# Kernel tuning notes

Measured on AMD Instinct MI355X. Metric: run time of the kernel, lower is better.

Reference implementation:

```python
import jax, jax.numpy as jnp
import numpy as np

B, T, D_IN, H1, H2 = 32, 2048, 1024, 512, 32


def setup_inputs() -> dict:
    key = jax.random.key(0)
    ks = jax.random.split(key, 8)
    avf_out = jax.random.normal(ks[0], (B, T, D_IN), dtype=jnp.float32)
    # seq_len in [1, T] so every sample has a non-empty slice (matches torch usage)
    seq_len = jax.random.randint(ks[1], (B,), 1, T + 1, dtype=jnp.int32)
    s = 0.02
    W1 = jax.random.normal(ks[2], (D_IN, H1), dtype=jnp.float32) * s
    b1 = jnp.zeros((H1,), dtype=jnp.float32)
    W2 = jax.random.normal(ks[3], (H1, H2), dtype=jnp.float32) * s
    b2 = jnp.zeros((H2,), dtype=jnp.float32)
    W3 = jax.random.normal(ks[4], (H2, 1), dtype=jnp.float32) * s
    b3 = jnp.zeros((1,), dtype=jnp.float32)
    return {"avf_out": avf_out, "W1": W1, "b1": b1, "W2": W2, "b2": b2,
            "W3": W3, "b3": b3, "seq_len": seq_len}


def reference(avf_out, W1, b1, W2, b2, W3, b3, seq_len):
    h = jax.nn.relu(jnp.einsum('btd,dh->bth', avf_out, W1) + b1)
    h = jnp.einsum('bth,hk->btk', h, W2) + b2
    logits = jax.nn.sigmoid(jnp.einsum('btk,ko->bto', h, W3) + b3)[..., 0]  # [B, T]
    # ragged per-sample top-k (k = seq_len//16 + 1 over first seq_len entries) + mean,
    # vectorized via masked descending sort + cumsum (no per-sample loop)
    Tn = logits.shape[1]
    valid = jnp.arange(Tn)[None, :] < seq_len[:, None]            # [B, T]
    NEG = jnp.float32(-1.0)  # below sigmoid range, so padded slots never enter top-k
    masked = jnp.where(valid, logits, NEG)
    sorted_desc = -jnp.sort(-masked, axis=1)                      # [B, T] descending
    csum = jnp.cumsum(sorted_desc, axis=1)
    k = seq_len // 16 + 1                                         # k <= seq_len always
    topk_sum = jnp.take_along_axis(csum, (k - 1)[:, None].astype(jnp.int32), axis=1)[:, 0]
    return topk_sum / k.astype(logits.dtype)                      # [B]
```

## Files before the change

kernel.cpp:

```cpp
#include <hip/hip_runtime.h>

typedef __bf16 bf16;
typedef __bf16 bf16x4 __attribute__((ext_vector_type(4)));
typedef __bf16 bf16x8 __attribute__((ext_vector_type(8)));
typedef float f32x4 __attribute__((ext_vector_type(4)));

#define M_TOT 65536
#define K_TOT 1024
#define N_TOT 512
#define T_SEQ 2048
#define NB 32

__device__ __forceinline__ void async16(const void* g, void* l) {
    __builtin_amdgcn_global_load_lds(
        (const __attribute__((address_space(1))) unsigned int*)g,
        (__attribute__((address_space(3))) unsigned int*)l, 16, 0, 0);
}

__global__ __launch_bounds__(256) void transpose_w1(const float* __restrict__ W1,
                                                    bf16* __restrict__ W1T) {
    __shared__ float tile[32][33];
    const int t = threadIdx.x;
    const int k0 = blockIdx.x * 32;
    const int n0 = blockIdx.y * 32;
#pragma unroll
    for (int p = 0; p < 4; p++) {
        int kl = p * 8 + (t >> 5);
        int nl = t & 31;
        tile[kl][nl] = W1[(k0 + kl) * 512 + n0 + nl];
    }
    __syncthreads();
#pragma unroll
    for (int p = 0; p < 4; p++) {
        int nl = p * 8 + (t >> 5);
        int kl = t & 31;
        W1T[(n0 + nl) * 1024 + k0 + kl] = (bf16)tile[kl][nl];
    }
}

__global__ __launch_bounds__(512) void make_v(const float* __restrict__ W2,
                                              const float* __restrict__ b2,
                                              const float* __restrict__ W3,
                                              const float* __restrict__ b3,
                                              float* __restrict__ v) {
    const int t = threadIdx.x;
    float s = 0.f;
#pragma unroll
    for (int c = 0; c < 32; c++) s += W2[t * 32 + c] * W3[c];
    v[t] = s;
    if (t == 0) {
        float cc = b3[0];
        for (int c = 0; c < 32; c++) cc += b2[c] * W3[c];
        v[512] = cc;
    }
}

__device__ __forceinline__ int sw_idx(int row, int e) {
    return row * 64 + ((((e >> 3) ^ (row & 7))) << 3) + (e & 7);
}

__global__ __launch_bounds__(512, 1) void gemm_fused(const float* __restrict__ A,
                                                     const bf16* __restrict__ W1T,
                                                     const float* __restrict__ b1,
                                                     const float* __restrict__ v,
                                                     float* __restrict__ logits) {
    __shared__ bf16 smem[(128 + 512) * 64];
    bf16* As = smem;
    bf16* Bs = smem + 128 * 64;

    const int t = threadIdx.x;
    const int wave = t >> 6, lane = t & 63;
    const int q = lane >> 4, l15 = lane & 15;
    const int wm = wave >> 2, wn = wave & 3;
    const int m0 = blockIdx.x * 128;

    const int arow = t >> 2;
    const int ae0  = (t & 3) * 16;
    const float* agp = A + (size_t)(m0 + arow) * K_TOT + ae0;

    const int bl_row   = wave * 64 + (lane >> 3);
    const int bl_chunk = (lane & 7) ^ ((lane >> 3) & 7);
    const bf16* bgp = W1T + (size_t)bl_row * K_TOT + bl_chunk * 8;

    f32x4 acc[4][8] = {};

#pragma unroll 1
    for (int k0 = 0; k0 < K_TOT; k0 += 64) {
        float4 av[4];
#pragma unroll
        for (int p = 0; p < 4; p++) av[p] = *(const float4*)(agp + k0 + p * 4);

        __syncthreads();

#pragma unroll
        for (int j = 0; j < 8; j++)
            async16(bgp + k0 + (size_t)j * 8 * K_TOT,
                    Bs + (wave * 64 + j * 8) * 64);

        {
            bf16x8 c0, c1;
            c0[0] = (bf16)av[0].x; c0[1] = (bf16)av[0].y;
            c0[2] = (bf16)av[0].z; c0[3] = (bf16)av[0].w;
            c0[4] = (bf16)av[1].x; c0[5] = (bf16)av[1].y;
            c0[6] = (bf16)av[1].z; c0[7] = (bf16)av[1].w;
            c1[0] = (bf16)av[2].x; c1[1] = (bf16)av[2].y;
            c1[2] = (bf16)av[2].z; c1[3] = (bf16)av[2].w;
            c1[4] = (bf16)av[3].x; c1[5] = (bf16)av[3].y;
            c1[6] = (bf16)av[3].z; c1[7] = (bf16)av[3].w;
            *(bf16x8*)(&As[sw_idx(arow, ae0)])     = c0;
            *(bf16x8*)(&As[sw_idx(arow, ae0 + 8)]) = c1;
        }

        __syncthreads();

#pragma unroll
        for (int kk = 0; kk < 64; kk += 32) {
            const int e = kk + q * 8;
            bf16x8 af[4], bfr[8];
#pragma unroll
            for (int mi = 0; mi < 4; mi++) {
                int row = wm * 64 + mi * 16 + l15;
                af[mi] = *(const bf16x8*)(&As[sw_idx(row, e)]);
            }
#pragma unroll
            for (int ni = 0; ni < 8; ni++) {
                int n = wn * 128 + ni * 16 + l15;
                bfr[ni] = *(const bf16x8*)(&Bs[sw_idx(n, e)]);
            }
#pragma unroll
            for (int mi = 0; mi < 4; mi++)
#pragma unroll
                for (int ni = 0; ni < 8; ni++)
                    acc[mi][ni] = __builtin_amdgcn_mfma_f32_16x16x32_bf16(
                        af[mi], bfr[ni], acc[mi][ni], 0, 0, 0);
        }
    }

    float bb[8], vv[8];
#pragma unroll
    for (int ni = 0; ni < 8; ni++) {
        int col = wn * 128 + ni * 16 + l15;
        bb[ni] = b1[col];
        vv[ni] = v[col];
    }
    const float cconst = v[512];

    __syncthreads();
    float* part = (float*)smem;

#pragma unroll
    for (int mi = 0; mi < 4; mi++) {
#pragma unroll
        for (int r = 0; r < 4; r++) {
            float s = 0.f;
#pragma unroll
            for (int ni = 0; ni < 8; ni++)
                s += fmaxf(acc[mi][ni][r] + bb[ni], 0.f) * vv[ni];
            s += __shfl_xor(s, 1);
            s += __shfl_xor(s, 2);
            s += __shfl_xor(s, 4);
            s += __shfl_xor(s, 8);
            if (l15 == 0) {
                int row = wm * 64 + mi * 16 + q * 4 + r;
                part[row * 4 + wn] = s;
            }
        }
    }
    __syncthreads();
    if (t < 128) {
        float s = part[t * 4] + part[t * 4 + 1] + part[t * 4 + 2] + part[t * 4 + 3] + cconst;
        logits[m0 + t] = 1.f / (1.f + __expf(-s));
    }
}

__global__ __launch_bounds__(256) void topk_mean(const float* __restrict__ logits,
                                                 const int* __restrict__ seq_len,
                                                 float* __restrict__ out) {
    __shared__ float vals[T_SEQ];
    __shared__ int redi[4];
    __shared__ float redf[4];
    const int b = blockIdx.x, t = threadIdx.x;
    const int lane = t & 63, wave = t >> 6;
    const int L = seq_len[b];
    const int k = (L >> 4) + 1;
    const float* p = logits + b * T_SEQ;
    for (int i = t; i < L; i += 256) vals[i] = p[i];
    __syncthreads();

    unsigned lo = 0u, hi = 0x3f800000u;
    while (lo < hi) {
        unsigned mid = lo + ((hi - lo + 1) >> 1);
        float thr = __uint_as_float(mid);
        int cnt = 0;
        for (int i = t; i < L; i += 256) cnt += (vals[i] >= thr) ? 1 : 0;
#pragma unroll
        for (int m = 32; m >= 1; m >>= 1) cnt += __shfl_xor(cnt, m);
        if (lane == 0) redi[wave] = cnt;
        __syncthreads();
        int total = redi[0] + redi[1] + redi[2] + redi[3];
        __syncthreads();
        if (total >= k) lo = mid; else hi = mid - 1;
    }
    const float thr = __uint_as_float(lo);

    int cnt = 0; float sum = 0.f;
    for (int i = t; i < L; i += 256) {
        float x = vals[i];
        if (x > thr) { cnt += 1; sum += x; }
    }
#pragma unroll
    for (int m = 32; m >= 1; m >>= 1) { cnt += __shfl_xor(cnt, m); sum += __shfl_xor(sum, m); }
    if (lane == 0) { redi[wave] = cnt; redf[wave] = sum; }
    __syncthreads();
    if (t == 0) {
        int cgt = redi[0] + redi[1] + redi[2] + redi[3];
        float sgt = redf[0] + redf[1] + redf[2] + redf[3];
        out[b] = (sgt + (float)(k - cgt) * thr) / (float)k;
    }
}

extern "C" void kernel_launch(void* const* d_in, const int* in_sizes, int n_in,
                              void* d_out, int out_size, void* d_ws, size_t ws_size,
                              hipStream_t stream) {
    const float* avf = (const float*)d_in[0];
    const float* W1  = (const float*)d_in[1];
    const float* b1  = (const float*)d_in[2];
    const float* W2  = (const float*)d_in[3];
    const float* b2  = (const float*)d_in[4];
    const float* W3  = (const float*)d_in[5];
    const float* b3  = (const float*)d_in[6];
    const int* seq_len = (const int*)d_in[7];
    float* out = (float*)d_out;

    char* ws = (char*)d_ws;
    bf16*  W1T    = (bf16*)ws;
    float* v      = (float*)(ws + (1 << 20));
    float* logits = (float*)(ws + (1 << 20) + 4096);

    transpose_w1<<<dim3(32, 16), 256, 0, stream>>>(W1, W1T);
    make_v<<<1, 512, 0, stream>>>(W2, b2, W3, b3, v);
    gemm_fused<<<512, 512, 0, stream>>>(avf, W1T, b1, v, logits);
    topk_mean<<<NB, 256, 0, stream>>>(logits, seq_len, out);
}
```

Baseline: 458.0 us.

## Double-buffer LDS tiles in fused GEMM and prefetch next K-step during MFMA

Splits shared memory into two buffers so the global loads of A and the async B loads for the next K-step are issued before the MFMA work on the current buffer. This drops one barrier per iteration. A loads are regrouped so four adjacent threads read contiguous 16-float spans and write bf16x4 chunks into the swizzled layout. Launch bounds now request two blocks per CU. The doubled LDS footprint (160KB) likely still allows only one block, while the tighter register budget risks spilling the 128-float accumulator.

```diff
diff --git a/kernel.cpp b/kernel.cpp
--- a/kernel.cpp
+++ b/kernel.cpp
@@ -5,7 +5,6 @@
 typedef __bf16 bf16x8 __attribute__((ext_vector_type(8)));
 typedef float f32x4 __attribute__((ext_vector_type(4)));
 
-#define M_TOT 65536
 #define K_TOT 1024
 #define N_TOT 512
 #define T_SEQ 2048
@@ -56,17 +55,15 @@
 }
 
 __device__ __forceinline__ int sw_idx(int row, int e) {
-    return row * 64 + ((((e >> 3) ^ (row & 7))) << 3) + (e & 7);
-}
-
-__global__ __launch_bounds__(512, 1) void gemm_fused(const float* __restrict__ A,
+    return row * 64 + (((e >> 3) ^ (row & 7)) << 3) + (e & 7);
+}
+
+__global__ __launch_bounds__(512, 2) void gemm_fused(const float* __restrict__ A,
                                                      const bf16* __restrict__ W1T,
                                                      const float* __restrict__ b1,
                                                      const float* __restrict__ v,
                                                      float* __restrict__ logits) {
-    __shared__ bf16 smem[(128 + 512) * 64];
-    bf16* As = smem;
-    bf16* Bs = smem + 128 * 64;
+    __shared__ bf16 smem[2][(128 + 512) * 64];
 
     const int t = threadIdx.x;
     const int wave = t >> 6, lane = t & 63;
@@ -74,66 +71,75 @@
     const int wm = wave >> 2, wn = wave & 3;
     const int m0 = blockIdx.x * 128;
 
-    const int arow = t >> 2;
-    const int ae0  = (t & 3) * 16;
-    const float* agp = A + (size_t)(m0 + arow) * K_TOT + ae0;
-
-    const int bl_row   = wave * 64 + (lane >> 3);
+    const int arow = t >> 2, ac = t & 3;
+    const float* agp = A + (size_t)(m0 + arow) * K_TOT + ac * 4;
+
+    const int bl_row = wave * 64 + (lane >> 3);
     const int bl_chunk = (lane & 7) ^ ((lane >> 3) & 7);
     const bf16* bgp = W1T + (size_t)bl_row * K_TOT + bl_chunk * 8;
 
     f32x4 acc[4][8] = {};
-
-#pragma unroll 1
-    for (int k0 = 0; k0 < K_TOT; k0 += 64) {
-        float4 av[4];
-#pragma unroll
-        for (int p = 0; p < 4; p++) av[p] = *(const float4*)(agp + k0 + p * 4);
-
-        __syncthreads();
-
+    float4 av[4];
+
+    auto loadA = [&](int k0) {
+#pragma unroll
+        for (int p = 0; p < 4; p++) av[p] = *(const float4*)(agp + k0 + p * 16);
+    };
+    auto asyncB = [&](int k0, int b) {
+        bf16* bs = smem[b] + 128 * 64;
 #pragma unroll
         for (int j = 0; j < 8; j++)
-            async16(bgp + k0 + (size_t)j * 8 * K_TOT,
-                    Bs + (wave * 64 + j * 8) * 64);
-
-        {
-            bf16x8 c0, c1;
-            c0[0] = (bf16)av[0].x; c0[1] = (bf16)av[0].y;
-            c0[2] = (bf16)av[0].z; c0[3] = (bf16)av[0].w;
-            c0[4] = (bf16)av[1].x; c0[5] = (bf16)av[1].y;
-            c0[6] = (bf16)av[1].z; c0[7] = (bf16)av[1].w;
-            c1[0] = (bf16)av[2].x; c1[1] = (bf16)av[2].y;
-            c1[2] = (bf16)av[2].z; c1[3] = (bf16)av[2].w;
-            c1[4] = (bf16)av[3].x; c1[5] = (bf16)av[3].y;
-            c1[6] = (bf16)av[3].z; c1[7] = (bf16)av[3].w;
-            *(bf16x8*)(&As[sw_idx(arow, ae0)])     = c0;
-            *(bf16x8*)(&As[sw_idx(arow, ae0 + 8)]) = c1;
-        }
-
-        __syncthreads();
-
+            async16(bgp + k0 + (size_t)j * 8 * K_TOT, bs + (wave * 64 + j * 8) * 64);
+    };
+    auto writeA = [&](int b) {
+        bf16* as = smem[b];
+#pragma unroll
+        for (int p = 0; p < 4; p++) {
+            bf16x4 w;
+            w[0] = (bf16)av[p].x; w[1] = (bf16)av[p].y;
+            w[2] = (bf16)av[p].z; w[3] = (bf16)av[p].w;
+            int chunk = 2 * p + (ac >> 1);
+            int idx = arow * 64 + ((chunk ^ (arow & 7)) << 3) + (ac & 1) * 4;
+            *(bf16x4*)(&as[idx]) = w;
+        }
+    };
+    auto mfma_phase = [&](int b) {
+        const bf16* as = smem[b];
+        const bf16* bs = smem[b] + 128 * 64;
 #pragma unroll
         for (int kk = 0; kk < 64; kk += 32) {
             const int e = kk + q * 8;
-            bf16x8 af[4], bfr[8];
-#pragma unroll
-            for (int mi = 0; mi < 4; mi++) {
-                int row = wm * 64 + mi * 16 + l15;
-                af[mi] = *(const bf16x8*)(&As[sw_idx(row, e)]);
-            }
-#pragma unroll
-            for (int ni = 0; ni < 8; ni++) {
-                int n = wn * 128 + ni * 16 + l15;
-                bfr[ni] = *(const bf16x8*)(&Bs[sw_idx(n, e)]);
-            }
+            bf16x8 af[4], bfv[8];
+#pragma unroll
+            for (int mi = 0; mi < 4; mi++)
+                af[mi] = *(const bf16x8*)(&as[sw_idx(wm * 64 + mi * 16 + l15, e)]);
+#pragma unroll
+            for (int ni = 0; ni < 8; ni++)
+                bfv[ni] = *(const bf16x8*)(&bs[sw_idx(wn * 128 + ni * 16 + l15, e)]);
 #pragma unroll
             for (int mi = 0; mi < 4; mi++)
 #pragma unroll
                 for (int ni = 0; ni < 8; ni++)
                     acc[mi][ni] = __builtin_amdgcn_mfma_f32_16x16x32_bf16(
-                        af[mi], bfr[ni], acc[mi][ni], 0, 0, 0);
-        }
+                        af[mi], bfv[ni], acc[mi][ni], 0, 0, 0);
+        }
+    };
+
+    loadA(0);
+    asyncB(0, 0);
+    writeA(0);
+    __syncthreads();
+
+#pragma unroll 1
+    for (int k = 0; k < 16; k++) {
+        const int buf = k & 1, nxt = buf ^ 1;
+        if (k < 15) {
+            loadA((k + 1) * 64);
+            asyncB((k + 1) * 64, nxt);
+        }
+        mfma_phase(buf);
+        if (k < 15) writeA(nxt);
+        __syncthreads();
     }
 
     float bb[8], vv[8];
```

After: 426.0 us. -7.0%, faster.

## Split GEMM over N into four blocks with double-buffered B and direct A loads

Applied to the files above, without the earlier changes.

The fused GEMM kernel is restructured so each block computes only a 128-column slice of the hidden layer instead of all 512 columns. This raises the grid to 2048 blocks of 256 threads, with up to 3 blocks per CU. B tiles are now double-buffered with async LDS loads, and A is read straight from global memory into registers, skipping LDS staging. A new kernel sums the four per-slice partial dot products and applies the sigmoid. The trade-off is that the fp32 input A is read four times from global memory, and an extra launch plus a partial buffer round-trip are added.

```diff
diff --git a/kernel.cpp b/kernel.cpp
--- a/kernel.cpp
+++ b/kernel.cpp
@@ -56,97 +56,84 @@
 }
 
 __device__ __forceinline__ int sw_idx(int row, int e) {
-    return row * 64 + ((((e >> 3) ^ (row & 7))) << 3) + (e & 7);
-}
-
-__global__ __launch_bounds__(512, 1) void gemm_fused(const float* __restrict__ A,
-                                                     const bf16* __restrict__ W1T,
-                                                     const float* __restrict__ b1,
-                                                     const float* __restrict__ v,
-                                                     float* __restrict__ logits) {
-    __shared__ bf16 smem[(128 + 512) * 64];
-    bf16* As = smem;
-    bf16* Bs = smem + 128 * 64;
+    return row * 64 + (((e >> 3) ^ (row & 7)) << 3) + (e & 7);
+}
+
+__global__ __launch_bounds__(256, 3) void gemm_part(const float* __restrict__ A,
+                                                    const bf16* __restrict__ W1T,
+                                                    const float* __restrict__ b1,
+                                                    const float* __restrict__ v,
+                                                    float* __restrict__ partial) {
+    __shared__ bf16 Bs[2][128 * 64];
+    __shared__ float part[128][2];
 
     const int t = threadIdx.x;
     const int wave = t >> 6, lane = t & 63;
-    const int q = lane >> 4, l15 = lane & 15;
-    const int wm = wave >> 2, wn = wave & 3;
-    const int m0 = blockIdx.x * 128;
-
-    const int arow = t >> 2;
-    const int ae0  = (t & 3) * 16;
-    const float* agp = A + (size_t)(m0 + arow) * K_TOT + ae0;
-
-    const int bl_row   = wave * 64 + (lane >> 3);
-    const int bl_chunk = (lane & 7) ^ ((lane >> 3) & 7);
-    const bf16* bgp = W1T + (size_t)bl_row * K_TOT + bl_chunk * 8;
-
-    f32x4 acc[4][8] = {};
+    const int lq = lane >> 4, l15 = lane & 15;
+    const int wm = wave >> 1, wn = wave & 1;
+    const int nq = blockIdx.x;
+    const int m0 = blockIdx.y * 128;
+    const int n0 = nq * 128;
+
+    const int blr = (lane >> 3);
+    const int blc = (lane & 7) ^ blr;
+    const bf16* bgp = W1T + (size_t)(n0 + wave * 32 + blr) * K_TOT + blc * 8;
+
+    const float* agp = A + (size_t)(m0 + wm * 64 + l15) * K_TOT + lq * 8;
+
+    f32x4 acc[4][4] = {};
+
+    auto asyncB = [&](int k0, int b) {
+        bf16* bs = Bs[b];
+#pragma unroll
+        for (int j = 0; j < 4; j++)
+            async16(bgp + k0 + (size_t)j * 8 * K_TOT,
+                    bs + (wave * 32 + j * 8) * 64);
+    };
+
+    asyncB(0, 0);
+    __syncthreads();
 
 #pragma unroll 1
-    for (int k0 = 0; k0 < K_TOT; k0 += 64) {
-        float4 av[4];
-#pragma unroll
-        for (int p = 0; p < 4; p++) av[p] = *(const float4*)(agp + k0 + p * 4);
-
+    for (int k = 0; k < 16; k++) {
+        const int buf = k & 1;
+        const int k0 = k * 64;
+        if (k < 15) asyncB(k0 + 64, buf ^ 1);
+#pragma unroll
+        for (int kk = 0; kk < 64; kk += 32) {
+            bf16x8 af[4];
+#pragma unroll
+            for (int mi = 0; mi < 4; mi++) {
+                const float* p = agp + (size_t)(mi * 16) * K_TOT + k0 + kk;
+                float4 x = *(const float4*)(p);
+                float4 y = *(const float4*)(p + 4);
+                bf16x8 f;
+                f[0] = (bf16)x.x; f[1] = (bf16)x.y; f[2] = (bf16)x.z; f[3] = (bf16)x.w;
+                f[4] = (bf16)y.x; f[5] = (bf16)y.y; f[6] = (bf16)y.z; f[7] = (bf16)y.w;
+                af[mi] = f;
+            }
+            bf16x8 bfv[4];
+            const int e = kk + lq * 8;
+#pragma unroll
+            for (int ni = 0; ni < 4; ni++)
+                bfv[ni] = *(const bf16x8*)(&Bs[buf][sw_idx(wn * 64 + ni * 16 + l15, e)]);
+#pragma unroll
+            for (int mi = 0; mi < 4; mi++)
+#pragma unroll
+                for (int ni = 0; ni < 4; ni++)
+                    acc[mi][ni] = __builtin_amdgcn_mfma_f32_16x16x32_bf16(
+                        af[mi], bfv[ni], acc[mi][ni], 0, 0, 0);
+        }
         __syncthreads();
-
-#pragma unroll
-        for (int j = 0; j < 8; j++)
-            async16(bgp + k0 + (size_t)j * 8 * K_TOT,
-                    Bs + (wave * 64 + j * 8) * 64);
-
-        {
-            bf16x8 c0, c1;
-            c0[0] = (bf16)av[0].x; c0[1] = (bf16)av[0].y;
-            c0[2] = (bf16)av[0].z; c0[3] = (bf16)av[0].w;
-            c0[4] = (bf16)av[1].x; c0[5] = (bf16)av[1].y;
-            c0[6] = (bf16)av[1].z; c0[7] = (bf16)av[1].w;
-            c1[0] = (bf16)av[2].x; c1[1] = (bf16)av[2].y;
-            c1[2] = (bf16)av[2].z; c1[3] = (bf16)av[2].w;
-            c1[4] = (bf16)av[3].x; c1[5] = (bf16)av[3].y;
-            c1[6] = (bf16)av[3].z; c1[7] = (bf16)av[3].w;
-            *(bf16x8*)(&As[sw_idx(arow, ae0)])     = c0;
-            *(bf16x8*)(&As[sw_idx(arow, ae0 + 8)]) = c1;
-        }
-
-        __syncthreads();
-
-#pragma unroll
-        for (int kk = 0; kk < 64; kk += 32) {
-            const int e = kk + q * 8;
-            bf16x8 af[4], bfr[8];
-#pragma unroll
-            for (int mi = 0; mi < 4; mi++) {
-                int row = wm * 64 + mi * 16 + l15;
-                af[mi] = *(const bf16x8*)(&As[sw_idx(row, e)]);
-            }
-#pragma unroll
-            for (int ni = 0; ni < 8; ni++) {
-                int n = wn * 128 + ni * 16 + l15;
-                bfr[ni] = *(const bf16x8*)(&Bs[sw_idx(n, e)]);
-            }
-#pragma unroll
-            for (int mi = 0; mi < 4; mi++)
-#pragma unroll
-                for (int ni = 0; ni < 8; ni++)
-                    acc[mi][ni] = __builtin_amdgcn_mfma_f32_16x16x32_bf16(
-                        af[mi], bfr[ni], acc[mi][ni], 0, 0, 0);
-        }
-    }
-
-    float bb[8], vv[8];
-#pragma unroll
-    for (int ni = 0; ni < 8; ni++) {
-        int col = wn * 128 + ni * 16 + l15;
+    }
+
+    float bb[4], vv[4];
+#pragma unroll
+    for (int ni = 0; ni < 4; ni++) {
+        int col = n0 + wn * 64 + ni * 16 + l15;
         bb[ni] = b1[col];
         vv[ni] = v[col];
     }
-    const float cconst = v[512];
-
-    __syncthreads();
-    float* part = (float*)smem;
 
 #pragma unroll
     for (int mi = 0; mi < 4; mi++) {
@@ -154,23 +141,28 @@
         for (int r = 0; r < 4; r++) {
             float s = 0.f;
 #pragma unroll
-            for (int ni = 0; ni < 8; ni++)
+            for (int ni = 0; ni < 4; ni++)
                 s += fmaxf(acc[mi][ni][r] + bb[ni], 0.f) * vv[ni];
             s += __shfl_xor(s, 1);
             s += __shfl_xor(s, 2);
             s += __shfl_xor(s, 4);
             s += __shfl_xor(s, 8);
-            if (l15 == 0) {
-                int row = wm * 64 + mi * 16 + q * 4 + r;
-                part[row * 4 + wn] = s;
-            }
+            if (l15 == 0) part[wm * 64 + mi * 16 + lq * 4 + r][wn] = s;
         }
     }
     __syncthreads();
-    if (t < 128) {
-        float s = part[t * 4] + part[t * 4 + 1] + part[t * 4 + 2] + part[t * 4 + 3] + cconst;
-        logits[m0 + t] = 1.f / (1.f + __expf(-s));
-    }
+    if (t < 128)
+        partial[(size_t)nq * M_TOT + m0 + t] = part[t][0] + part[t][1];
+}
+
+__global__ __launch_bounds__(256) void sum_sigmoid(const float* __restrict__ partial,
+                                                   const float* __restrict__ v,
+                                                   float* __restrict__ logits) {
+    const int m = blockIdx.x * 256 + threadIdx.x;
+    const float c = v[512];
+    float s = partial[m] + partial[M_TOT + m] + partial[2 * M_TOT + m] +
+              partial[3 * M_TOT + m] + c;
+    logits[m] = 1.f / (1.f + __expf(-s));
 }
 
 __global__ __launch_bounds__(256) void topk_mean(const float* __restrict__ logits,
@@ -235,10 +227,12 @@
     char* ws = (char*)d_ws;
     bf16*  W1T    = (bf16*)ws;
     float* v      = (float*)(ws + (1 << 20));
-    float* logits = (float*)(ws + (1 << 20) + 4096);
+    float* logits = (float*)(ws + (1 << 20) + (1 << 16));
+    float* partial= (float*)(ws + (2 << 20));
 
     transpose_w1<<<dim3(32, 16), 256, 0, stream>>>(W1, W1T);
     make_v<<<1, 512, 0, stream>>>(W2, b2, W3, b3, v);
-    gemm_fused<<<512, 512, 0, stream>>>(avf, W1T, b1, v, logits);
+    gemm_part<<<dim3(4, 512), 256, 0, stream>>>(avf, W1T, b1, v, partial);
+    sum_sigmoid<<<M_TOT / 256, 256, 0, stream>>>(partial, v, logits);
     topk_mean<<<NB, 256, 0, stream>>>(logits, seq_len, out);
 }
```

New measurement: 582.4 us. +27.2%, slower.
